# Kernel tuning notes

Hardware: AMD Instinct MI355X
Metric: run time of the kernel (lower is better)

## Reference

```python
import jax, jax.numpy as jnp
import numpy as np

# Brevitas-style binary quant constants:
# SignedBinaryWeightPerTensorConst -> sign(w) * 0.1 (const per-tensor scale)
# SignedBinaryActPerTensorConst    -> sign(x) * 1.0
W_SCALE = 0.1
A_SCALE = 1.0
EMBED = 9984  # 128 channels * 78 spatial


def _sign(x):
    return jnp.where(x >= 0, 1.0, -1.0).astype(x.dtype)


def bin_w(w):
    # binary weight quant with straight-through estimator
    q = W_SCALE * _sign(w)
    return w + jax.lax.stop_gradient(q - w)


def bin_act(x):
    # QuantHardTanh with binary act quant: forward = sign(x)*A_SCALE,
    # backward = hardtanh gradient (clip to [-1, 1])
    ht = jnp.clip(x, -1.0, 1.0)
    q = A_SCALE * _sign(x)
    return ht + jax.lax.stop_gradient(q - ht)


def scale_bias(x, s, b):
    # QuantScaleBias: per-channel scale (binary-quantized) + bias
    sq = bin_w(s)
    if x.ndim == 3:  # (N, C, L)
        return x * sq[None, :, None] + b[None, :, None]
    return x * sq[None, :] + b[None, :]


def conv1d(x, w, dilation):
    return jax.lax.conv_general_dilated(
        x, w, window_strides=(1,), padding='VALID',
        rhs_dilation=(dilation,), dimension_numbers=('NCH', 'OIH', 'NCH'))


def maxpool1d(x, k):
    return jax.lax.reduce_window(x, -jnp.inf, jax.lax.max,
                                 (1, 1, k), (1, 1, k), 'VALID')


def forward(x, s0, b0, w1, s1, b1, w2, s2, b2, w3, s3, b3,
            w4, s4, b4, w5, s5, b5, fw1, s6, b6, fw2, s7, b7):
    x = scale_bias(x, s0, b0)                     # (N,3,16000)
    x = conv1d(x, bin_w(w1), 1)                   # (N,64,15960)
    x = bin_act(scale_bias(x, s1, b1))
    x = maxpool1d(x, 3)                           # (N,64,5320)
    x = conv1d(x, bin_w(w2), 2)                   # (N,64,5240)
    x = bin_act(scale_bias(x, s2, b2))
    x = maxpool1d(x, 3)                           # (N,64,1746)
    x = conv1d(x, bin_w(w3), 2)                   # (N,128,1666)
    x = bin_act(scale_bias(x, s3, b3))
    x = maxpool1d(x, 3)                           # (N,128,555)
    x = conv1d(x, bin_w(w4), 2)                   # (N,128,475)
    x = bin_act(scale_bias(x, s4, b4))
    x = maxpool1d(x, 3)                           # (N,128,158)
    x = conv1d(x, bin_w(w5), 2)                   # (N,128,78)
    x = bin_act(scale_bias(x, s5, b5))
    x = x.reshape(-1, EMBED)                      # (N,9984)
    x = x @ bin_w(fw1).T                          # (N,1024)
    x = bin_act(scale_bias(x, s6, b6))
    x = x @ bin_w(fw2).T                          # (N,1000)
    x = scale_bias(x, s7, b7)
    return x


def setup_inputs() -> dict:
    key = jax.random.key(0)
    ks = jax.random.split(key, 24)
    n = lambda k, shp: jax.random.normal(k, shp, dtype=jnp.float32) * 0.05
    return {
        'x': jax.random.normal(ks[0], (64, 3, 16000), dtype=jnp.float32),
        's0': n(ks[1], (3,)), 'b0': n(ks[2], (3,)),
        'w1': n(ks[3], (64, 3, 41)), 's1': n(ks[4], (64,)), 'b1': n(ks[5], (64,)),
        'w2': n(ks[6], (64, 64, 41)), 's2': n(ks[7], (64,)), 'b2': n(ks[8], (64,)),
        'w3': n(ks[9], (128, 64, 41)), 's3': n(ks[10], (128,)), 'b3': n(ks[11], (128,)),
        'w4': n(ks[12], (128, 128, 41)), 's4': n(ks[13], (128,)), 'b4': n(ks[14], (128,)),
        'w5': n(ks[15], (128, 128, 41)), 's5': n(ks[16], (128,)), 'b5': n(ks[17], (128,)),
        'fw1': n(ks[18], (1024, EMBED)), 's6': n(ks[19], (1024,)), 'b6': n(ks[20], (1024,)),
        'fw2': n(ks[21], (1000, 1024)), 's7': n(ks[22], (1000,)), 'b7': n(ks[23], (1000,)),
    }


def reference(x, s0, b0, w1, s1, b1, w2, s2, b2, w3, s3, b3,
              w4, s4, b4, w5, s5, b5, fw1, s6, b6, fw2, s7, b7):
    return forward(x, s0, b0, w1, s1, b1, w2, s2, b2, w3, s3, b3,
                   w4, s4, b4, w5, s5, b5, fw1, s6, b6, fw2, s7, b7)
```

## Files before the change

kernel.cpp:

```cpp
#include <hip/hip_runtime.h>
#include <cstdint>

typedef unsigned long long u64;
typedef unsigned int u32;

#define L_X 16000
#define NB  64
#define P1  5320
#define P2  1746
#define P3  555
#define P4  158
#define C5  78

__device__ __forceinline__ void chain64(float& A, u64 u) {
    u32 w = (u32)u;
    #pragma unroll
    for (int j = 0; j < 32; ++j)
        A = __fadd_rn(A, __uint_as_float(0x3DCCCCCDu | ((w << (31 - j)) & 0x80000000u)));
    w = (u32)(u >> 32);
    #pragma unroll
    for (int j = 0; j < 32; ++j)
        A = __fadd_rn(A, __uint_as_float(0x3DCCCCCDu | ((w << (31 - j)) & 0x80000000u)));
}

#define SEG0 123
#define SEG1 (SEG0 + 2624)
#define SEG2 (SEG1 + 5248)
#define SEG3 (SEG2 + 10496)
#define SEG4 (SEG3 + 10496)
#define SEG5 (SEG4 + 159744)
#define SEG6 (SEG5 + 16000)

__device__ __forceinline__ void pack_conv(const float* w, u64* wT, int t, int Co, int CIW) {
    int co = t % Co;
    int rem = t / Co;
    int h = rem % CIW;
    int k = rem / CIW;
    int CI = CIW * 64;
    u64 word = 0;
    for (int c = 0; c < 64; ++c)
        if (w[((size_t)co * CI + h * 64 + c) * 41 + k] < 0.f) word |= 1ull << c;
    wT[t] = word;
}

__global__ void pack_all(const float* __restrict__ w1, const float* __restrict__ w2,
                         const float* __restrict__ w3, const float* __restrict__ w4,
                         const float* __restrict__ w5, const float* __restrict__ fw1,
                         const float* __restrict__ fw2,
                         u64* __restrict__ w1k, u64* __restrict__ w2T,
                         u64* __restrict__ w3T, u64* __restrict__ w4T,
                         u64* __restrict__ w5T, u64* __restrict__ fw1T,
                         u64* __restrict__ fw2T) {
    int tid = blockIdx.x * blockDim.x + threadIdx.x;
    if (tid < SEG0) {
        int ci = tid % 3;
        int k = tid / 3;
        u64 word = 0;
        for (int co = 0; co < 64; ++co)
            if (w1[(co * 3 + ci) * 41 + k] < 0.f) word |= 1ull << co;
        w1k[k * 4 + ci] = word;
    } else if (tid < SEG1) {
        pack_conv(w2, w2T, tid - SEG0, 64, 1);
    } else if (tid < SEG2) {
        pack_conv(w3, w3T, tid - SEG1, 128, 1);
    } else if (tid < SEG3) {
        pack_conv(w4, w4T, tid - SEG2, 128, 2);
    } else if (tid < SEG4) {
        pack_conv(w5, w5T, tid - SEG3, 128, 2);
    } else if (tid < SEG5) {
        int t = tid - SEG4;
        int row = t & 1023;
        int j = t >> 10;
        const float* base = fw1 + (size_t)row * 9984 + j * 64;
        u64 word = 0;
        for (int c = 0; c < 64; ++c)
            if (base[c] < 0.f) word |= 1ull << c;
        fw1T[t] = word;
    } else if (tid < SEG6) {
        int t = tid - SEG5;
        int row = t % 1000;
        int j = t / 1000;
        const float* base = fw2 + (size_t)row * 1024 + j * 64;
        u64 word = 0;
        for (int c = 0; c < 64; ++c)
            if (base[c] < 0.f) word |= 1ull << c;
        fw2T[t] = word;
    }
}

__global__ void repack_a5(const u64* __restrict__ a5, u64* __restrict__ a5F) {
    int t = blockIdx.x * blockDim.x + threadIdx.x;
    if (t >= NB * 156) return;
    int j = t % 156;
    int n = t / 156;
    u64 word = 0;
    #pragma unroll
    for (int c = 0; c < 64; ++c) {
        int jj = j * 64 + c;
        int chan = jj / 78;
        int tp = jj - chan * 78;
        u64 src = a5[((size_t)n * C5 + tp) * 2 + (chan >> 6)];
        word |= ((src >> (chan & 63)) & 1ull) << c;
    }
    a5F[t] = word;
}

__global__ __launch_bounds__(64) void conv1_s(
        const float* __restrict__ x, const u64* __restrict__ w1k,
        const float* __restrict__ s0, const float* __restrict__ b0,
        const float* __restrict__ s1, const float* __restrict__ b1,
        u64* __restrict__ a1) {
    __shared__ float yl[3][232];
    __shared__ float s1l[64], b1l[64];
    int lane = threadIdx.x;
    int qb = blockIdx.x * 64;
    int n = blockIdx.y;

    #pragma unroll
    for (int ci = 0; ci < 3; ++ci) {
        float sq = (s0[ci] < 0.f) ? -0.1f : 0.1f;
        float bb = b0[ci];
        const float* xp = x + ((size_t)n * 3 + ci) * L_X;
        for (int i = lane; i < 232; i += 64) {
            int t = 3 * qb + i;
            t = (t < L_X) ? t : (L_X - 1);
            float xsb = __fadd_rn(__fmul_rn(xp[t], sq), bb);
            yl[ci][i] = __fmul_rn(xsb, 0.1f);
        }
    }
    s1l[lane] = s1[lane];
    b1l[lane] = b1[lane];
    __syncthreads();

    int q = qb + lane;
    bool valid = q < P1;
    int base = 3 * lane;
    u64 word = 0;

    #pragma unroll 1
    for (int tile = 0; tile < 4; ++tile) {
        float S[16][3];
        #pragma unroll
        for (int c = 0; c < 16; ++c)
            #pragma unroll
            for (int r = 0; r < 3; ++r) S[c][r] = 0.f;

        #pragma unroll 1
        for (int k = 0; k < 41; ++k) {
            float y0[3], y1[3], y2[3];
            #pragma unroll
            for (int r = 0; r < 3; ++r) {
                y0[r] = yl[0][base + k + r];
                y1[r] = yl[1][base + k + r];
                y2[r] = yl[2][base + k + r];
            }
            u32 t0 = (u32)(w1k[k * 4 + 0] >> (tile * 16));
            u32 t1 = (u32)(w1k[k * 4 + 1] >> (tile * 16));
            u32 t2 = (u32)(w1k[k * 4 + 2] >> (tile * 16));
            #pragma unroll
            for (int c = 0; c < 16; ++c) {
                float wf0 = __uint_as_float(0x3F800000u | (((t0 >> c) & 1u) << 31));
                float wf1 = __uint_as_float(0x3F800000u | (((t1 >> c) & 1u) << 31));
                float wf2 = __uint_as_float(0x3F800000u | (((t2 >> c) & 1u) << 31));
                #pragma unroll
                for (int r = 0; r < 3; ++r) {
                    float A = __fmul_rn(y0[r], wf0);
                    A = __fmaf_rn(y1[r], wf1, A);
                    A = __fmaf_rn(y2[r], wf2, A);
                    S[c][r] = __fadd_rn(S[c][r], A);
                }
            }
        }
        #pragma unroll
        for (int c = 0; c < 16; ++c) {
            int co = tile * 16 + c;
            float sq1 = (s1l[co] < 0.f) ? -0.1f : 0.1f;
            float bb1 = b1l[co];
            bool neg = true;
            #pragma unroll
            for (int r = 0; r < 3; ++r) {
                float pre = __fadd_rn(__fmul_rn(S[c][r], sq1), bb1);
                neg = neg && (pre < 0.f);
            }
            word |= (u64)(neg ? 1 : 0) << co;
        }
    }
    if (valid) a1[(size_t)n * P1 + q] = word;
}

template <int CIW, int POOLK>
__global__ void bconv_g(const u64* __restrict__ abits_in, const u64* __restrict__ wT,
                        const float* __restrict__ s, const float* __restrict__ b,
                        u64* __restrict__ abits_out, int Lin, int Lq, double G) {
    constexpr int BITS = 41 * CIW * 64;
    int q = blockIdx.x;
    int n = blockIdx.y;
    int co = threadIdx.x;
    int Co = blockDim.x;
    int wave = co >> 6;
    int CoW = Co >> 6;
    float sqf = (s[co] < 0.f) ? -0.1f : 0.1f;
    float bf  = b[co];
    const u64* wp = wT + co;
    const u64* ap = abits_in + ((size_t)n * Lin + (size_t)POOLK * q) * CIW;

    int pc[POOLK];
    #pragma unroll
    for (int r = 0; r < POOLK; ++r) pc[r] = 0;
    #pragma unroll 1
    for (int k = 0; k < 41; ++k) {
        u64 wk[CIW];
        #pragma unroll
        for (int h = 0; h < CIW; ++h) wk[h] = wp[((size_t)k * CIW + h) * Co];
        const u64* ak = ap + (size_t)(2 * k) * CIW;
        #pragma unroll
        for (int r = 0; r < POOLK; ++r) {
            #pragma unroll
            for (int h = 0; h < CIW; ++h)
                pc[r] += (int)__popcll(ak[r * CIW + h] ^ wk[h]);
        }
    }
    const double vv = (double)0.1f * (double)0.1f;
    double svv = (sqf < 0.f) ? -vv : vv;
    double bd = (double)bf;
    bool negr[POOLK], flagr[POOLK], nn[POOLK];
    #pragma unroll
    for (int r = 0; r < POOLK; ++r) {
        double pre = (double)(BITS - 2 * pc[r]) * svv + bd;
        negr[r] = (pre < 0.0);
        flagr[r] = (fabs(pre) < G);
        nn[r] = (pre > G);
    }
    #pragma unroll
    for (int r = 0; r < POOLK; ++r) {
        bool other_nn = false;
        #pragma unroll
        for (int r2 = 0; r2 < POOLK; ++r2)
            if (r2 != r) other_nn = other_nn || nn[r2];
        bool need = flagr[r] && !other_nn;
        if (__ballot(need) != 0ull) {
            float S = 0.f;
            #pragma unroll 1
            for (int k = 0; k < 41; ++k) {
                float A = 0.f;
                #pragma unroll
                for (int h = 0; h < CIW; ++h) {
                    u64 u = ap[(size_t)(2 * k + r) * CIW + h]
                          ^ wp[((size_t)k * CIW + h) * Co];
                    chain64(A, u);
                }
                S = __fadd_rn(S, A);
            }
            negr[r] = (__fadd_rn(__fmul_rn(S, sqf), bf) < 0.f);
        }
    }
    bool neg = true;
    #pragma unroll
    for (int r = 0; r < POOLK; ++r) neg = neg && negr[r];
    u64 word = __ballot(neg);
    if ((co & 63) == 0) abits_out[((size_t)n * Lq + q) * CoW + wave] = word;
}

__global__ __launch_bounds__(64) void fc1_k(
        const u64* __restrict__ a5F, const u64* __restrict__ fw1T,
        const float* __restrict__ s6, const float* __restrict__ b6,
        u64* __restrict__ y6b) {
    int g = blockIdx.x;
    int n = blockIdx.y;
    int lane = threadIdx.x;
    int row = g * 64 + lane;
    float S = 0.f;
    #pragma unroll 1
    for (int j = 0; j < 156; ++j) {
        u64 u = a5F[(size_t)n * 156 + j] ^ fw1T[(size_t)j * 1024 + row];
        chain64(S, u);
    }
    float pre = __fadd_rn(__fmul_rn(S, (s6[row] < 0.f) ? -0.1f : 0.1f), b6[row]);
    u64 word = __ballot(pre < 0.f);
    if (lane == 0) y6b[n * 16 + g] = word;
}

__global__ void fc2_k(const u64* __restrict__ y6b, const u64* __restrict__ fw2T,
                      const float* __restrict__ s7, const float* __restrict__ b7,
                      float* __restrict__ out) {
    int t = blockIdx.x * blockDim.x + threadIdx.x;
    if (t >= NB * 1000) return;
    int r = t % 1000;
    int n = t / 1000;
    float S = 0.f;
    #pragma unroll 1
    for (int j = 0; j < 16; ++j) {
        u64 u = y6b[n * 16 + j] ^ fw2T[j * 1000 + r];
        chain64(S, u);
    }
    out[t] = __fadd_rn(__fmul_rn(S, (s7[r] < 0.f) ? -0.1f : 0.1f), b7[r]);
}

extern "C" void kernel_launch(void* const* d_in, const int* in_sizes, int n_in,
                              void* d_out, int out_size, void* d_ws, size_t ws_size,
                              hipStream_t stream) {
    const float* x   = (const float*)d_in[0];
    const float* s0  = (const float*)d_in[1];
    const float* b0  = (const float*)d_in[2];
    const float* w1  = (const float*)d_in[3];
    const float* s1  = (const float*)d_in[4];
    const float* b1  = (const float*)d_in[5];
    const float* w2  = (const float*)d_in[6];
    const float* s2  = (const float*)d_in[7];
    const float* b2  = (const float*)d_in[8];
    const float* w3  = (const float*)d_in[9];
    const float* s3  = (const float*)d_in[10];
    const float* b3  = (const float*)d_in[11];
    const float* w4  = (const float*)d_in[12];
    const float* s4  = (const float*)d_in[13];
    const float* b4  = (const float*)d_in[14];
    const float* w5  = (const float*)d_in[15];
    const float* s5  = (const float*)d_in[16];
    const float* b5  = (const float*)d_in[17];
    const float* fw1 = (const float*)d_in[18];
    const float* s6  = (const float*)d_in[19];
    const float* b6  = (const float*)d_in[20];
    const float* fw2 = (const float*)d_in[21];
    const float* s7  = (const float*)d_in[22];
    const float* b7  = (const float*)d_in[23];

    u64* p = (u64*)d_ws;
    u64* w1kb = p; p += 41 * 4;
    u64* w2T  = p; p += 41 * 64;
    u64* w3T  = p; p += 41 * 128;
    u64* w4T  = p; p += 82 * 128;
    u64* w5T  = p; p += 82 * 128;
    u64* fw1T = p; p += 156 * 1024;
    u64* fw2T = p; p += 16 * 1000;
    u64* a1   = p; p += (size_t)NB * P1;
    u64* a2   = p; p += (size_t)NB * P2;
    u64* a3   = p; p += (size_t)NB * P3 * 2;
    u64* a4   = p; p += (size_t)NB * P4 * 2;
    u64* a5   = p; p += (size_t)NB * C5 * 2;
    u64* a5F  = p; p += (size_t)NB * 156;
    u64* y6b  = p; p += (size_t)NB * 16;

    const double G64  = 2.0e-4;
    const double G128 = 5.0e-4;

    pack_all<<<(SEG6 + 255) / 256, 256, 0, stream>>>(
        w1, w2, w3, w4, w5, fw1, fw2, w1kb, w2T, w3T, w4T, w5T, fw1T, fw2T);

    conv1_s<<<dim3((P1 + 63) / 64, NB), 64, 0, stream>>>(x, w1kb, s0, b0, s1, b1, a1);
    bconv_g<1, 3><<<dim3(P2, NB), 64, 0, stream>>>(a1, w2T, s2, b2, a2, P1, P2, G64);
    bconv_g<1, 3><<<dim3(P3, NB), 128, 0, stream>>>(a2, w3T, s3, b3, a3, P2, P3, G64);
    bconv_g<2, 3><<<dim3(P4, NB), 128, 0, stream>>>(a3, w4T, s4, b4, a4, P3, P4, G128);
    bconv_g<2, 1><<<dim3(C5, NB), 128, 0, stream>>>(a4, w5T, s5, b5, a5, P4, C5, G128);
    repack_a5<<<(NB * 156 + 255) / 256, 256, 0, stream>>>(a5, a5F);
    fc1_k<<<dim3(16, NB), 64, 0, stream>>>(a5F, fw1T, s6, b6, y6b);
    fc2_k<<<(NB * 1000 + 255) / 256, 256, 0, stream>>>(y6b, fw2T, s7, b7, (float*)d_out);
}
```

Baseline: 993.2 us.

## Defer exact float-order recompute of borderline outputs to a worklist fix-up kernel

Instead of having a whole wavefront run the slow serial float-accumulation path whenever any lane lands near the sign threshold, each borderline (n,q,co) is appended to a global worklist via an atomic counter. A separate fix-up kernel per layer recomputes only those entries and flips the output bit with an atomic XOR when the exact result differs from the popcount guess. This removes wavefront divergence stalls in the main conv kernels, at the cost of extra kernel launches, atomics, and a memset of the counters.

```diff
diff --git a/kernel.cpp b/kernel.cpp
--- a/kernel.cpp
+++ b/kernel.cpp
@@ -191,7 +191,8 @@
 template <int CIW, int POOLK>
 __global__ void bconv_g(const u64* __restrict__ abits_in, const u64* __restrict__ wT,
                         const float* __restrict__ s, const float* __restrict__ b,
-                        u64* __restrict__ abits_out, int Lin, int Lq, double G) {
+                        u64* __restrict__ abits_out, int Lin, int Lq, double G,
+                        u32* __restrict__ wl, u32* __restrict__ wl_count, u32 wl_cap) {
     constexpr int BITS = 41 * CIW * 64;
     int q = blockIdx.x;
     int n = blockIdx.y;
@@ -223,7 +224,7 @@
     const double vv = (double)0.1f * (double)0.1f;
     double svv = (sqf < 0.f) ? -vv : vv;
     double bd = (double)bf;
-    bool negr[POOLK], flagr[POOLK], nn[POOLK];
+    bool negr[POOLK], flagr[POOLK], nn[POOLK], need[POOLK];
     #pragma unroll
     for (int r = 0; r < POOLK; ++r) {
         double pre = (double)(BITS - 2 * pc[r]) * svv + bd;
@@ -231,14 +232,28 @@
         flagr[r] = (fabs(pre) < G);
         nn[r] = (pre > G);
     }
+    bool need_any = false;
     #pragma unroll
     for (int r = 0; r < POOLK; ++r) {
         bool other_nn = false;
         #pragma unroll
         for (int r2 = 0; r2 < POOLK; ++r2)
             if (r2 != r) other_nn = other_nn || nn[r2];
-        bool need = flagr[r] && !other_nn;
-        if (__ballot(need) != 0ull) {
+        need[r] = flagr[r] && !other_nn;
+        need_any = need_any || need[r];
+    }
+    bool handled = false;
+    if (need_any) {
+        u32 idx = atomicAdd(wl_count, 1u);
+        if (idx < wl_cap) {
+            wl[idx] = ((u32)n << 18) | ((u32)q << 7) | (u32)co;
+            handled = true;
+        }
+    }
+    #pragma unroll
+    for (int r = 0; r < POOLK; ++r) {
+        bool nr = need[r] && !handled;
+        if (__ballot(nr) != 0ull) {
             float S = 0.f;
             #pragma unroll 1
             for (int k = 0; k < 41; ++k) {
@@ -251,7 +266,7 @@
                 }
                 S = __fadd_rn(S, A);
             }
-            negr[r] = (__fadd_rn(__fmul_rn(S, sqf), bf) < 0.f);
+            if (nr) negr[r] = (__fadd_rn(__fmul_rn(S, sqf), bf) < 0.f);
         }
     }
     bool neg = true;
@@ -259,6 +274,88 @@
     for (int r = 0; r < POOLK; ++r) neg = neg && negr[r];
     u64 word = __ballot(neg);
     if ((co & 63) == 0) abits_out[((size_t)n * Lq + q) * CoW + wave] = word;
+}
+
+template <int CIW, int POOLK>
+__global__ void bfix(const u64* __restrict__ abits_in, const u64* __restrict__ wT,
+                     const float* __restrict__ s, const float* __restrict__ b,
+                     u64* __restrict__ abits_out, int Lin, int Lq, double G,
+                     const u32* __restrict__ wl, const u32* __restrict__ wl_count,
+                     u32 wl_cap, int Co) {
+    constexpr int BITS = 41 * CIW * 64;
+    u32 cnt = *wl_count;
+    if (cnt > wl_cap) cnt = wl_cap;
+    for (u32 i = blockIdx.x * blockDim.x + threadIdx.x; i < cnt;
+         i += gridDim.x * blockDim.x) {
+        u32 e = wl[i];
+        int co = e & 127;
+        int q  = (e >> 7) & 2047;
+        int n  = (int)(e >> 18);
+        const u64* wp = wT + co;
+        const u64* ap = abits_in + ((size_t)n * Lin + (size_t)POOLK * q) * CIW;
+        float sqf = (s[co] < 0.f) ? -0.1f : 0.1f;
+        float bf  = b[co];
+        int pc[POOLK];
+        #pragma unroll
+        for (int r = 0; r < POOLK; ++r) pc[r] = 0;
+        #pragma unroll 1
+        for (int k = 0; k < 41; ++k) {
+            u64 wk[CIW];
+            #pragma unroll
+            for (int h = 0; h < CIW; ++h) wk[h] = wp[((size_t)k * CIW + h) * Co];
+            const u64* ak = ap + (size_t)(2 * k) * CIW;
+            #pragma unroll
+            for (int r = 0; r < POOLK; ++r) {
+                #pragma unroll
+                for (int h = 0; h < CIW; ++h)
+                    pc[r] += (int)__popcll(ak[r * CIW + h] ^ wk[h]);
+            }
+        }
+        const double vv = (double)0.1f * (double)0.1f;
+        double svv = (sqf < 0.f) ? -vv : vv;
+        double bd = (double)bf;
+        bool negr[POOLK], flagr[POOLK], nn[POOLK];
+        #pragma unroll
+        for (int r = 0; r < POOLK; ++r) {
+            double pre = (double)(BITS - 2 * pc[r]) * svv + bd;
+            negr[r] = (pre < 0.0);
+            flagr[r] = (fabs(pre) < G);
+            nn[r] = (pre > G);
+        }
+        bool guess = true;
+        #pragma unroll
+        for (int r = 0; r < POOLK; ++r) guess = guess && negr[r];
+        #pragma unroll 1
+        for (int r = 0; r < POOLK; ++r) {
+            bool other_nn = false;
+            #pragma unroll
+            for (int r2 = 0; r2 < POOLK; ++r2)
+                if (r2 != r) other_nn = other_nn || nn[r2];
+            if (flagr[r] && !other_nn) {
+                float S = 0.f;
+                #pragma unroll 1
+                for (int k = 0; k < 41; ++k) {
+                    float A = 0.f;
+                    #pragma unroll
+                    for (int h = 0; h < CIW; ++h) {
+                        u64 u = ap[(size_t)(2 * k + r) * CIW + h]
+                              ^ wp[((size_t)k * CIW + h) * Co];
+                        chain64(A, u);
+                    }
+                    S = __fadd_rn(S, A);
+                }
+                negr[r] = (__fadd_rn(__fmul_rn(S, sqf), bf) < 0.f);
+            }
+        }
+        bool truebit = true;
+        #pragma unroll
+        for (int r = 0; r < POOLK; ++r) truebit = truebit && negr[r];
+        if (truebit != guess) {
+            int wave = co >> 6;
+            int CoW = Co >> 6;
+            atomicXor(&abits_out[((size_t)n * Lq + q) * CoW + wave], 1ull << (co & 63));
+        }
+    }
 }
 
 __global__ __launch_bounds__(64) void fc1_k(
@@ -339,18 +436,43 @@
     u64* a5   = p; p += (size_t)NB * C5 * 2;
     u64* a5F  = p; p += (size_t)NB * 156;
     u64* y6b  = p; p += (size_t)NB * 16;
+    u32* cnts = (u32*)p; p += 8;
+    u32* wl2 = (u32*)p; p += 512 * 1024 / 2;
+    u32* wl3 = (u32*)p; p += 256 * 1024 / 2;
+    u32* wl4 = (u32*)p; p += 128 * 1024 / 2;
+    u32* wl5 = (u32*)p; p += 32 * 1024 / 2;
+    const u32 CAP2 = 512 * 1024, CAP3 = 256 * 1024, CAP4 = 128 * 1024, CAP5 = 32 * 1024;
 
     const double G64  = 2.0e-4;
     const double G128 = 5.0e-4;
 
+    hipMemsetAsync(cnts, 0, 4 * sizeof(u32), stream);
+
     pack_all<<<(SEG6 + 255) / 256, 256, 0, stream>>>(
         w1, w2, w3, w4, w5, fw1, fw2, w1kb, w2T, w3T, w4T, w5T, fw1T, fw2T);
 
     conv1_s<<<dim3((P1 + 63) / 64, NB), 64, 0, stream>>>(x, w1kb, s0, b0, s1, b1, a1);
-    bconv_g<1, 3><<<dim3(P2, NB), 64, 0, stream>>>(a1, w2T, s2, b2, a2, P1, P2, G64);
-    bconv_g<1, 3><<<dim3(P3, NB), 128, 0, stream>>>(a2, w3T, s3, b3, a3, P2, P3, G64);
-    bconv_g<2, 3><<<dim3(P4, NB), 128, 0, stream>>>(a3, w4T, s4, b4, a4, P3, P4, G128);
-    bconv_g<2, 1><<<dim3(C5, NB), 128, 0, stream>>>(a4, w5T, s5, b5, a5, P4, C5, G128);
+
+    bconv_g<1, 3><<<dim3(P2, NB), 64, 0, stream>>>(a1, w2T, s2, b2, a2, P1, P2, G64,
+                                                   wl2, cnts + 0, CAP2);
+    bfix<1, 3><<<256, 256, 0, stream>>>(a1, w2T, s2, b2, a2, P1, P2, G64,
+                                        wl2, cnts + 0, CAP2, 64);
+
+    bconv_g<1, 3><<<dim3(P3, NB), 128, 0, stream>>>(a2, w3T, s3, b3, a3, P2, P3, G64,
+                                                    wl3, cnts + 1, CAP3);
+    bfix<1, 3><<<256, 256, 0, stream>>>(a2, w3T, s3, b3, a3, P2, P3, G64,
+                                        wl3, cnts + 1, CAP3, 128);
+
+    bconv_g<2, 3><<<dim3(P4, NB), 128, 0, stream>>>(a3, w4T, s4, b4, a4, P3, P4, G128,
+                                                    wl4, cnts + 2, CAP4);
+    bfix<2, 3><<<256, 256, 0, stream>>>(a3, w4T, s4, b4, a4, P3, P4, G128,
+                                        wl4, cnts + 2, CAP4, 128);
+
+    bconv_g<2, 1><<<dim3(C5, NB), 128, 0, stream>>>(a4, w5T, s5, b5, a5, P4, C5, G128,
+                                                    wl5, cnts + 3, CAP5);
+    bfix<2, 1><<<128, 256, 0, stream>>>(a4, w5T, s5, b5, a5, P4, C5, G128,
+                                        wl5, cnts + 3, CAP5, 128);
+
     repack_a5<<<(NB * 156 + 255) / 256, 256, 0, stream>>>(a5, a5F);
     fc1_k<<<dim3(16, NB), 64, 0, stream>>>(a5F, fw1T, s6, b6, y6b);
     fc2_k<<<(NB * 1000 + 255) / 256, 256, 0, stream>>>(y6b, fw2T, s7, b7, (float*)d_out);
```

Result: slower. 1.110 ms (+11.8%).
